# Optimization experiments

Hardware: AMD Instinct MI355X
Metric: run time of the kernel (lower is better)

## Reference

```python
import jax, jax.numpy as jnp
import numpy as np

B = 16384
R, N_NODES, K, N_LAYERS, LATENT = 5, 68, 32, 3, 68


def setup_inputs() -> dict:
    key = jax.random.key(0)
    ks = jax.random.split(key, 6)
    z = jax.random.normal(ks[0], (B, LATENT), dtype=jnp.float32)
    adjacency = jax.random.randint(ks[1], (N_NODES, K), 0, N_NODES)
    # init_fc weights stored as [latent, n_nodes] so forward is z @ fc_w[r] + fc_b[r]
    fc_w = jax.random.normal(ks[2], (R, LATENT, N_NODES), dtype=jnp.float32) * 0.1
    fc_b = jax.random.normal(ks[3], (R, N_NODES), dtype=jnp.float32) * 0.1
    gcn_w = jax.random.normal(ks[4], (R, N_LAYERS, N_NODES, K), dtype=jnp.float32) * 0.1
    gcn_b = jax.random.normal(ks[5], (R, N_LAYERS, N_NODES), dtype=jnp.float32) * 0.1
    return {"z": z, "adjacency": adjacency, "fc_w": fc_w, "fc_b": fc_b,
            "gcn_w": gcn_w, "gcn_b": gcn_b}


def _gcn_layer(x, adjacency, w, b):
    # x: [B, N]; adjacency: [N, K] int; w: [N, K]; b: [N]
    x_nb = x[:, adjacency]                      # [B, N, K] ragged-style gather
    val = jnp.einsum('bnk,nk->bn', x_nb, w) + b  # per-node weighted neighbor sum
    return jax.nn.sigmoid(val)


def reference(z, adjacency, fc_w, fc_b, gcn_w, gcn_b):
    b = z.shape[0]
    sc_sum = jnp.zeros((b, N_NODES, N_NODES), dtype=z.dtype)
    for r in range(R):
        x = z @ fc_w[r] + fc_b[r]               # init_fc[r]
        for l in range(N_LAYERS):
            x = _gcn_layer(x, adjacency, gcn_w[r, l], gcn_b[r, l])
        # rank-1 outer product per sample: bmm(x.unsqueeze(2), x.unsqueeze(1))
        sc_sum = sc_sum + x[:, :, None] * x[:, None, :]
    sc_sum = 0.5 * (sc_sum + jnp.swapaxes(sc_sum, 1, 2))
    return sc_sum.reshape(b, -1)
```

## Files before the change

kernel.cpp:

```cpp
#include <hip/hip_runtime.h>
#include <math.h>

#define R_ 5
#define NN 68
#define KK 32
#define NL 3
#define LAT 68
#define NSL 17
#define ROWQ (NN / 4)
#define NF4 ((NN * NN) / 4)
#define BBK2 16
#define LSTR 344

__global__ __launch_bounds__(128) void densify_k(
    const int* __restrict__ adj, const float* __restrict__ gw,
    float* __restrict__ wd) {
  const int rl = blockIdx.x;
  const int t = threadIdx.x;
  __shared__ float col[NN][NN + 4];
  for (int i = t; i < NN * (NN + 4); i += 128) (&col[0][0])[i] = 0.0f;
  __syncthreads();
  if (t < NN) {
    const int n = t;
    const int* ar = adj + n * KK;
    const float* wr = gw + ((size_t)rl * NN + n) * KK;
    for (int k = 0; k < KK; ++k) col[ar[k]][n] += wr[k];
  }
  __syncthreads();
  float* wout = wd + (size_t)rl * NN * NN;
  for (int i = t; i < NN * NN; i += 128) {
    const int m = i / NN, n = i - m * NN;
    wout[i] = col[m][n];
  }
}

__global__ __launch_bounds__(256) void ztr_k(const float* __restrict__ z,
                                             float* __restrict__ zT, int B) {
  const int t = threadIdx.x;
  const int b0 = blockIdx.x * 64;
  __shared__ float zls[64][LAT + 1];
  for (int idx = t; idx < 64 * ROWQ; idx += 256) {
    const int row = idx / ROWQ, q = idx - row * ROWQ;
    const float4 v =
        *reinterpret_cast<const float4*>(z + (size_t)(b0 + row) * LAT + 4 * q);
    zls[row][4 * q + 0] = v.x;
    zls[row][4 * q + 1] = v.y;
    zls[row][4 * q + 2] = v.z;
    zls[row][4 * q + 3] = v.w;
  }
  __syncthreads();
  for (int idx = t; idx < LAT * 64; idx += 256) {
    const int l = idx >> 6, bb = idx & 63;
    zT[(size_t)l * B + b0 + bb] = zls[bb][l];
  }
}

__global__ __launch_bounds__(256) void chain_k(
    const float* __restrict__ zT, const float* __restrict__ fc_w,
    const float* __restrict__ fc_b, const float* __restrict__ wd,
    const float* __restrict__ gb, float* __restrict__ X, int B, int nb) {
  const int t = threadIdx.x;
  const int lane = t & 63;
  const int w = __builtin_amdgcn_readfirstlane(t >> 6);
  const int n0 = w * NSL;
  const int r = blockIdx.x / nb;
  const int b0 = (blockIdx.x - r * nb) * 64;

  __shared__ float xs[NN][64];

  for (int idx = t; idx < NN * 64; idx += 256) {
    const int m = idx >> 6;
    xs[m][idx & 63] = zT[(size_t)m * B + b0 + (idx & 63)];
  }
  __syncthreads();

  float acc[NSL];

#pragma unroll 1
  for (int stage = 0; stage < 1 + NL; ++stage) {
    const float* wb = (stage == 0) ? fc_w + (size_t)r * LAT * NN
                                   : wd + (size_t)(r * NL + stage - 1) * NN * NN;
    const float* bias = (stage == 0) ? fc_b + r * NN
                                     : gb + (size_t)(r * NL + stage - 1) * NN;
#pragma unroll
    for (int j = 0; j < NSL; ++j) acc[j] = bias[n0 + j];

#pragma unroll 2
    for (int m = 0; m < NN; ++m) {
      const float xm = xs[m][lane];
      const float* wr = wb + m * NN + n0;
#pragma unroll
      for (int j = 0; j < NSL; ++j) acc[j] = fmaf(xm, wr[j], acc[j]);
    }
    if (stage > 0) {
#pragma unroll
      for (int j = 0; j < NSL; ++j)
        acc[j] = 1.0f / (1.0f + __expf(-acc[j]));
    }
    if (stage < NL) {
      __syncthreads();
#pragma unroll
      for (int j = 0; j < NSL; ++j) xs[n0 + j][lane] = acc[j];
      __syncthreads();
    }
  }

  float* Xb = X + ((size_t)r * NN + n0) * B + b0 + lane;
#pragma unroll
  for (int j = 0; j < NSL; ++j) Xb[(size_t)j * B] = acc[j];
}

__global__ __launch_bounds__(256) void outer_k(const float* __restrict__ X,
                                               float* __restrict__ out, int B) {
  const int t = threadIdx.x;
  const int b0 = blockIdx.x * BBK2;
  __shared__ float xls[BBK2 * LSTR];
  __shared__ float obuf[BBK2][4][NN];

  for (int idx = t; idx < R_ * NN * BBK2; idx += 256) {
    const int rn = idx >> 4, bb = idx & (BBK2 - 1);
    xls[bb * LSTR + rn] = X[(size_t)rn * B + b0 + bb];
  }
  __syncthreads();

  const int lane = t & 63;
  const int wv = t >> 6;
  const int bb = wv * 4 + (lane >> 4);
  const int c = lane & 15;
  const float* xb = &xls[bb * LSTR];

  float4 xj[R_], xj16[R_];
#pragma unroll
  for (int r = 0; r < R_; ++r)
    xj[r] = *reinterpret_cast<const float4*>(xb + r * NN + 4 * c);
#pragma unroll
  for (int r = 0; r < R_; ++r)
    xj16[r] = *reinterpret_cast<const float4*>(xb + r * NN + 64);

#pragma unroll 1
  for (int g = 0; g < 17; ++g) {
    float4 xi[R_];
#pragma unroll
    for (int r = 0; r < R_; ++r)
      xi[r] = *reinterpret_cast<const float4*>(xb + r * NN + 4 * g);
#pragma unroll
    for (int k = 0; k < 4; ++k) {
      float4 a = make_float4(0.f, 0.f, 0.f, 0.f);
#pragma unroll
      for (int r = 0; r < R_; ++r) {
        const float s = reinterpret_cast<const float*>(&xi[r])[k];
        a.x = fmaf(s, xj[r].x, a.x);
        a.y = fmaf(s, xj[r].y, a.y);
        a.z = fmaf(s, xj[r].z, a.z);
        a.w = fmaf(s, xj[r].w, a.w);
      }
      *reinterpret_cast<float4*>(&obuf[bb][k][4 * c]) = a;
      if (c == 0) {
        float4 e = make_float4(0.f, 0.f, 0.f, 0.f);
#pragma unroll
        for (int r = 0; r < R_; ++r) {
          const float s = reinterpret_cast<const float*>(&xi[r])[k];
          e.x = fmaf(s, xj16[r].x, e.x);
          e.y = fmaf(s, xj16[r].y, e.y);
          e.z = fmaf(s, xj16[r].z, e.z);
          e.w = fmaf(s, xj16[r].w, e.w);
        }
        *reinterpret_cast<float4*>(&obuf[bb][k][64]) = e;
      }
    }
    __syncthreads();

    const float4* ob4 = reinterpret_cast<const float4*>(&obuf[0][0][0]);
    for (int fg = t; fg < BBK2 * NN; fg += 256) {
      const int bb2 = fg / NN;
      const int rem = fg - bb2 * NN;
      const int i2 = rem / ROWQ, q2 = rem - i2 * ROWQ;
      reinterpret_cast<float4*>(out)[(size_t)(b0 + bb2) * NF4 +
                                     (size_t)(4 * g + i2) * ROWQ + q2] =
          ob4[fg];
    }
    __syncthreads();
  }
}

extern "C" void kernel_launch(void* const* d_in, const int* in_sizes, int n_in,
                              void* d_out, int out_size, void* d_ws, size_t ws_size,
                              hipStream_t stream) {
  const float* z    = (const float*)d_in[0];
  const int*   adj  = (const int*)  d_in[1];
  const float* fc_w = (const float*)d_in[2];
  const float* fc_b = (const float*)d_in[3];
  const float* gw   = (const float*)d_in[4];
  const float* gb   = (const float*)d_in[5];
  float* out = (float*)d_out;

  const int B = in_sizes[0] / LAT;
  float* wd = (float*)d_ws;
  float* zT = wd + R_ * NL * NN * NN;
  float* X  = zT + (size_t)LAT * B;

  const int nb = B / 64;

  densify_k<<<R_ * NL, 128, 0, stream>>>(adj, gw, wd);
  ztr_k<<<B / 64, 256, 0, stream>>>(z, zT, B);
  chain_k<<<R_ * nb, 256, 0, stream>>>(zT, fc_w, fc_b, wd, gb, X, B, nb);
  outer_k<<<B / BBK2, 256, 0, stream>>>(X, out, B);
}
```

Before: 147.1 us.

## Process two batch columns per thread in chain and write outer products directly

The chain kernel now gives each thread two batch samples (128 per block), so every weight load from global/scalar memory feeds two FMAs. This halves weight-read traffic per sample and also halves the block count. Separately, the outer-product kernel drops its shared-memory staging buffer and the two barriers per row group, writing float4 results straight to global memory with a partially unrolled loop. The trade-offs are higher register pressure in chain_k, and direct writes whose per-wavefront coalescing may differ from the staged copy.

```diff
diff --git a/kernel.cpp b/kernel.cpp
--- a/kernel.cpp
+++ b/kernel.cpp
@@ -58,23 +58,23 @@
 __global__ __launch_bounds__(256) void chain_k(
     const float* __restrict__ zT, const float* __restrict__ fc_w,
     const float* __restrict__ fc_b, const float* __restrict__ wd,
-    const float* __restrict__ gb, float* __restrict__ X, int B, int nb) {
+    const float* __restrict__ gb, float* __restrict__ X, int B, int ng) {
   const int t = threadIdx.x;
   const int lane = t & 63;
   const int w = __builtin_amdgcn_readfirstlane(t >> 6);
   const int n0 = w * NSL;
-  const int r = blockIdx.x / nb;
-  const int b0 = (blockIdx.x - r * nb) * 64;
-
-  __shared__ float xs[NN][64];
-
-  for (int idx = t; idx < NN * 64; idx += 256) {
-    const int m = idx >> 6;
-    xs[m][idx & 63] = zT[(size_t)m * B + b0 + (idx & 63)];
-  }
-  __syncthreads();
-
-  float acc[NSL];
+  const int r = blockIdx.x / ng;
+  const int b0 = (blockIdx.x - r * ng) * 128;
+
+  __shared__ float xs[NN][128];
+
+  for (int idx = t; idx < NN * 128; idx += 256) {
+    const int m = idx >> 7;
+    xs[m][idx & 127] = zT[(size_t)m * B + b0 + (idx & 127)];
+  }
+  __syncthreads();
+
+  float acc0[NSL], acc1[NSL];
 
 #pragma unroll 1
   for (int stage = 0; stage < 1 + NL; ++stage) {
@@ -83,31 +83,47 @@
     const float* bias = (stage == 0) ? fc_b + r * NN
                                      : gb + (size_t)(r * NL + stage - 1) * NN;
 #pragma unroll
-    for (int j = 0; j < NSL; ++j) acc[j] = bias[n0 + j];
+    for (int j = 0; j < NSL; ++j) {
+      acc0[j] = bias[n0 + j];
+      acc1[j] = acc0[j];
+    }
 
 #pragma unroll 2
     for (int m = 0; m < NN; ++m) {
-      const float xm = xs[m][lane];
+      const float xm0 = xs[m][lane];
+      const float xm1 = xs[m][lane + 64];
       const float* wr = wb + m * NN + n0;
 #pragma unroll
-      for (int j = 0; j < NSL; ++j) acc[j] = fmaf(xm, wr[j], acc[j]);
+      for (int j = 0; j < NSL; ++j) {
+        const float wv = wr[j];
+        acc0[j] = fmaf(xm0, wv, acc0[j]);
+        acc1[j] = fmaf(xm1, wv, acc1[j]);
+      }
     }
     if (stage > 0) {
 #pragma unroll
-      for (int j = 0; j < NSL; ++j)
-        acc[j] = 1.0f / (1.0f + __expf(-acc[j]));
+      for (int j = 0; j < NSL; ++j) {
+        acc0[j] = 1.0f / (1.0f + __expf(-acc0[j]));
+        acc1[j] = 1.0f / (1.0f + __expf(-acc1[j]));
+      }
     }
     if (stage < NL) {
       __syncthreads();
 #pragma unroll
-      for (int j = 0; j < NSL; ++j) xs[n0 + j][lane] = acc[j];
+      for (int j = 0; j < NSL; ++j) {
+        xs[n0 + j][lane] = acc0[j];
+        xs[n0 + j][lane + 64] = acc1[j];
+      }
       __syncthreads();
     }
   }
 
-  float* Xb = X + ((size_t)r * NN + n0) * B + b0 + lane;
-#pragma unroll
-  for (int j = 0; j < NSL; ++j) Xb[(size_t)j * B] = acc[j];
+  float* Xb = X + ((size_t)r * NN + n0) * B + b0;
+#pragma unroll
+  for (int j = 0; j < NSL; ++j) {
+    Xb[(size_t)j * B + lane] = acc0[j];
+    Xb[(size_t)j * B + 64 + lane] = acc1[j];
+  }
 }
 
 __global__ __launch_bounds__(256) void outer_k(const float* __restrict__ X,
@@ -115,7 +131,6 @@
   const int t = threadIdx.x;
   const int b0 = blockIdx.x * BBK2;
   __shared__ float xls[BBK2 * LSTR];
-  __shared__ float obuf[BBK2][4][NN];
 
   for (int idx = t; idx < R_ * NN * BBK2; idx += 256) {
     const int rn = idx >> 4, bb = idx & (BBK2 - 1);
@@ -137,7 +152,8 @@
   for (int r = 0; r < R_; ++r)
     xj16[r] = *reinterpret_cast<const float4*>(xb + r * NN + 64);
 
-#pragma unroll 1
+  float4* obase = reinterpret_cast<float4*>(out) + (size_t)(b0 + bb) * NF4;
+#pragma unroll 2
   for (int g = 0; g < 17; ++g) {
     float4 xi[R_];
 #pragma unroll
@@ -154,7 +170,7 @@
         a.z = fmaf(s, xj[r].z, a.z);
         a.w = fmaf(s, xj[r].w, a.w);
       }
-      *reinterpret_cast<float4*>(&obuf[bb][k][4 * c]) = a;
+      obase[(size_t)(4 * g + k) * ROWQ + c] = a;
       if (c == 0) {
         float4 e = make_float4(0.f, 0.f, 0.f, 0.f);
 #pragma unroll
@@ -165,21 +181,9 @@
           e.z = fmaf(s, xj16[r].z, e.z);
           e.w = fmaf(s, xj16[r].w, e.w);
         }
-        *reinterpret_cast<float4*>(&obuf[bb][k][64]) = e;
-      }
-    }
-    __syncthreads();
-
-    const float4* ob4 = reinterpret_cast<const float4*>(&obuf[0][0][0]);
-    for (int fg = t; fg < BBK2 * NN; fg += 256) {
-      const int bb2 = fg / NN;
-      const int rem = fg - bb2 * NN;
-      const int i2 = rem / ROWQ, q2 = rem - i2 * ROWQ;
-      reinterpret_cast<float4*>(out)[(size_t)(b0 + bb2) * NF4 +
-                                     (size_t)(4 * g + i2) * ROWQ + q2] =
-          ob4[fg];
-    }
-    __syncthreads();
+        obase[(size_t)(4 * g + k) * ROWQ + 16] = e;
+      }
+    }
   }
 }
 
@@ -199,10 +203,10 @@
   float* zT = wd + R_ * NL * NN * NN;
   float* X  = zT + (size_t)LAT * B;
 
-  const int nb = B / 64;
+  const int ng = B / 128;
 
   densify_k<<<R_ * NL, 128, 0, stream>>>(adj, gw, wd);
   ztr_k<<<B / 64, 256, 0, stream>>>(z, zT, B);
-  chain_k<<<R_ * nb, 256, 0, stream>>>(zT, fc_w, fc_b, wd, gb, X, B, nb);
+  chain_k<<<R_ * ng, 256, 0, stream>>>(zT, fc_w, fc_b, wd, gb, X, B, ng);
   outer_k<<<B / BBK2, 256, 0, stream>>>(X, out, B);
 }
```

Result: slower. 151.3 us (+2.8%).
